# Performance work log

Measured on AMD Instinct MI355X. Metric: run time of the kernel, lower is better.

## Reference

```python
import jax, jax.numpy as jnp
import numpy as np

TWN_THRESHOLD_FACTOR = 0.05
BN_EPS = 1e-5


def ternary_quantize(w):
    # threshold = 0.05 * max|w| (detached); q in {-1, 0, +1}
    t = TWN_THRESHOLD_FACTOR * jnp.max(jnp.abs(jax.lax.stop_gradient(w)))
    return (w > t).astype(w.dtype) - (w < -t).astype(w.dtype)


def conv2d(x, w, b):
    q = ternary_quantize(w)
    y = jax.lax.conv_general_dilated(x, q, (1, 1), 'VALID',
                                     dimension_numbers=('NCHW', 'OIHW', 'NCHW'))
    return y + b[None, :, None, None]


def linear(x, w, b):
    q = ternary_quantize(w)
    return x @ q.T + b


def bn_train(x, gamma, beta, axes):
    # training-mode batch norm (biased variance), matches torch BN in train()
    mean = jnp.mean(x, axis=axes, keepdims=True)
    var = jnp.var(x, axis=axes, keepdims=True)
    xhat = (x - mean) * jax.lax.rsqrt(var + BN_EPS)
    shape = [1] * x.ndim
    shape[1] = x.shape[1]
    return xhat * gamma.reshape(shape) + beta.reshape(shape)


def maxpool2(x):
    return jax.lax.reduce_window(x, -jnp.inf, jax.lax.max,
                                 (1, 1, 2, 2), (1, 1, 2, 2), 'VALID')


def setup_inputs() -> dict:
    key = jax.random.key(0)
    ks = jax.random.split(key, 8)
    B, Cin, H, W = 512, 1, 28, 28
    C1, C2, K = 64, 128, 5
    FLAT, F1, F2 = 4 * 4 * C2, 512, 10
    inp = {
        'x': jax.random.normal(ks[0], (B, Cin, H, W), jnp.float32),
        'conv1_w': jax.random.normal(ks[1], (C1, Cin, K, K), jnp.float32) * (1.0 / np.sqrt(Cin * K * K)),
        'conv1_b': jax.random.normal(ks[2], (C1,), jnp.float32) * 0.05,
        'bn1_g': jnp.ones((C1,), jnp.float32),
        'bn1_b': jnp.zeros((C1,), jnp.float32),
        'conv2_w': jax.random.normal(ks[3], (C2, C1, K, K), jnp.float32) * (1.0 / np.sqrt(C1 * K * K)),
        'conv2_b': jax.random.normal(ks[4], (C2,), jnp.float32) * 0.05,
        'bn2_g': jnp.ones((C2,), jnp.float32),
        'bn2_b': jnp.zeros((C2,), jnp.float32),
        'fc1_w': jax.random.normal(ks[5], (F1, FLAT), jnp.float32) * (1.0 / np.sqrt(FLAT)),
        'fc1_b': jax.random.normal(ks[6], (F1,), jnp.float32) * 0.05,
        'bn3_g': jnp.ones((F1,), jnp.float32),
        'bn3_b': jnp.zeros((F1,), jnp.float32),
        'fc2_w': jax.random.normal(ks[7], (F2, F1), jnp.float32) * (1.0 / np.sqrt(F1)),
        'fc2_b': jnp.zeros((F2,), jnp.float32),
    }
    return inp


def reference(x, conv1_w, conv1_b, bn1_g, bn1_b, conv2_w, conv2_b, bn2_g, bn2_b,
              fc1_w, fc1_b, bn3_g, bn3_b, fc2_w, fc2_b):
    h = jax.nn.relu(bn_train(conv2d(x, conv1_w, conv1_b), bn1_g, bn1_b, (0, 2, 3)))
    h = maxpool2(h)  # [B, 64, 12, 12]
    h = jax.nn.relu(bn_train(conv2d(h, conv2_w, conv2_b), bn2_g, bn2_b, (0, 2, 3)))
    h = maxpool2(h)  # [B, 128, 4, 4]
    h = h.reshape(h.shape[0], -1)  # [B, 2048]
    h = jax.nn.relu(bn_train(linear(h, fc1_w, fc1_b), bn3_g, bn3_b, (0,)))
    return linear(h, fc2_w, fc2_b)  # [B, 10]
```

## Files before the change

kernel.cpp:

```cpp
#include <hip/hip_runtime.h>
#include <stdint.h>

#define EPS 1e-5f

typedef short v8s __attribute__((ext_vector_type(8)));
typedef float v4f __attribute__((ext_vector_type(4)));

static const size_t W2F   = 8192;
static const size_t WF2F  = 212992;
static const size_t A_F   = 262144;
static const size_t PMN2F = 4980736;
static const size_t B_F   = 19136512;
static const size_t WF1T  = B_F + 1048576;

#define P_C1 1024
#define P_F2 1025
#define P_C2 1040
#define P_F1 1240

__device__ inline unsigned short f2bf(float f) {
    unsigned u = __float_as_uint(f);
    return (unsigned short)((u + 0x7FFF + ((u >> 16) & 1)) >> 16);
}

__device__ __forceinline__ void stage16(const unsigned short* g, unsigned short* l) {
    __builtin_amdgcn_global_load_lds(
        (const __attribute__((address_space(1))) unsigned int*)g,
        (__attribute__((address_space(3))) unsigned int*)l, 16, 0, 0);
}

__global__ void k_absz(const float* __restrict__ c1w, const float* __restrict__ c2w,
                       const float* __restrict__ f1w, const float* __restrict__ f2w,
                       float* __restrict__ wsf) {
    __shared__ float sm4[4];
    int blk = blockIdx.x;
    if (blk >= 384) {
        if (blk < 386) {
            int i = (blk - 384) * 256 + threadIdx.x + 16;
            if (i < 528) wsf[i] = 0.f;
        } else {
            int i = (blk - 386) * 256 + threadIdx.x + 1808;
            if (i < 2832) wsf[i] = 0.f;
        }
        return;
    }
    const float* w; int n; int nb; int bi; float* out;
    if (blk == 0)       { w = c1w; n = 1600;    nb = 1;   bi = 0;         out = wsf + P_C1; }
    else if (blk == 1)  { w = f2w; n = 5120;    nb = 1;   bi = 0;         out = wsf + P_F2; }
    else if (blk < 194) { w = c2w; n = 204800;  nb = 192; bi = blk - 2;   out = wsf + P_C2 + bi; }
    else                { w = f1w; n = 1048576; nb = 190; bi = blk - 194; out = wsf + P_F1 + bi; }
    float m = 0.f;
    for (int i = bi * 256 + threadIdx.x; i < n; i += nb * 256)
        m = fmaxf(m, fabsf(w[i]));
    #pragma unroll
    for (int o = 32; o; o >>= 1) m = fmaxf(m, __shfl_down(m, o));
    if ((threadIdx.x & 63) == 0) sm4[threadIdx.x >> 6] = m;
    __syncthreads();
    if (threadIdx.x == 0)
        *out = fmaxf(fmaxf(sm4[0], sm4[1]), fmaxf(sm4[2], sm4[3]));
}

__global__ __launch_bounds__(512) void k_mid(const float* __restrict__ x,
                                             const float* __restrict__ c1w,
                                             const float* __restrict__ c2w,
                                             const float* __restrict__ f1w,
                                             const float* __restrict__ f2w,
                                             float* __restrict__ wsf,
                                             unsigned* __restrict__ pmn1,
                                             unsigned short* __restrict__ w2u,
                                             unsigned short* __restrict__ wf1,
                                             float* __restrict__ wf2) {
    int blk = blockIdx.x;
    int tid = threadIdx.x;
    if (blk >= 512) {
        if (blk < 612) {
            float m = 0.f;
            for (int i = 0; i < 192; ++i) m = fmaxf(m, wsf[P_C2 + i]);
            float t = 0.05f * m;
            for (int i = (blk - 512) * 512 + tid; i < 204800; i += 100 * 512) {
                int j    = i & 7;
                int lane = (i >> 3) & 63;
                int mt   = (i >> 9) & 7;
                int ks   = (i >> 12) & 1;
                int p    = i >> 13;
                int c  = mt * 16 + (lane & 15);
                int ci = ks * 32 + (lane >> 4) * 8 + j;
                float v = c2w[c * 1600 + ci * 25 + p];
                w2u[i] = (v > t) ? (unsigned short)0x3F80
                                 : ((v < -t) ? (unsigned short)0xBF80 : (unsigned short)0);
            }
        } else if (blk < 868) {
            float m = 0.f;
            for (int i = 0; i < 190; ++i) m = fmaxf(m, wsf[P_F1 + i]);
            float t = 0.05f * m;
            for (int i = (blk - 612) * 512 + tid; i < 1048576; i += 256 * 512) {
                float v = f1w[i];
                unsigned short q = (v > t) ? (unsigned short)0x3F80
                                 : ((v < -t) ? (unsigned short)0xBF80 : (unsigned short)0);
                int f = i >> 11, k = i & 2047;
                int ft = f >> 4, fm = f & 15;
                int ks = k >> 5, kr = k & 31;
                int lane = (kr >> 3) * 16 + fm;
                wf1[((size_t)(ks * 32 + ft) * 64 + lane) * 8 + (kr & 7)] = q;
            }
        } else {
            float t = 0.05f * wsf[P_F2];
            for (int i = tid; i < 5120; i += 512) {
                float v = f2w[i];
                wf2[i] = (float)((v > t) - (v < -t));
            }
        }
        return;
    }
    __shared__ float xs[784];
    __shared__ float red[2][8][64];
    int b = blk;
    const float4* xim = (const float4*)(x + (size_t)b * 784);
    for (int i = tid; i < 196; i += 512) ((float4*)xs)[i] = xim[i];
    int c  = tid & 63;
    int wv = tid >> 6;
    float w[25];
    {
        float t = 0.05f * wsf[P_C1];
        const float* src = c1w + c * 25;
        #pragma unroll
        for (int k = 0; k < 25; ++k) {
            float v = src[k];
            w[k] = (float)((v > t) - (v < -t));
        }
    }
    __syncthreads();
    unsigned* ob = pmn1 + (size_t)b * 9216;
    float s = 0.f, s2 = 0.f;
    int ph = 0, pw = wv;
    for (int it = 0; it < 18; ++it) {
        const float* xp = xs + (ph * 2) * 28 + pw * 2;
        float win[36];
        #pragma unroll
        for (int i = 0; i < 6; ++i)
            #pragma unroll
            for (int j = 0; j < 3; ++j) {
                float2 t2 = *(const float2*)(xp + i * 28 + j * 2);
                win[i * 6 + j * 2] = t2.x; win[i * 6 + j * 2 + 1] = t2.y;
            }
        float v00 = 0.f, v01 = 0.f, v10 = 0.f, v11 = 0.f;
        #pragma unroll
        for (int i = 0; i < 5; ++i)
            #pragma unroll
            for (int j = 0; j < 5; ++j) {
                float wk = w[i * 5 + j];
                v00 = fmaf(win[i * 6 + j],           wk, v00);
                v01 = fmaf(win[i * 6 + j + 1],       wk, v01);
                v10 = fmaf(win[(i + 1) * 6 + j],     wk, v10);
                v11 = fmaf(win[(i + 1) * 6 + j + 1], wk, v11);
            }
        s  += v00 + v01 + v10 + v11;
        s2 += v00 * v00 + v01 * v01 + v10 * v10 + v11 * v11;
        float mx = fmaxf(fmaxf(v00, v01), fmaxf(v10, v11));
        float mn = fminf(fminf(v00, v01), fminf(v10, v11));
        ob[(ph * 12 + pw) * 64 + c] = ((unsigned)f2bf(mx) << 16) | (unsigned)f2bf(mn);
        pw += 8; if (pw >= 12) { pw -= 12; ++ph; }
    }
    red[0][wv][c] = s; red[1][wv][c] = s2;
    __syncthreads();
    if (tid < 64) {
        float S = 0.f, S2 = 0.f;
        #pragma unroll
        for (int i = 0; i < 8; ++i) { S += red[0][i][tid]; S2 += red[1][i][tid]; }
        atomicAdd(&wsf[16 + tid], S);
        atomicAdd(&wsf[80 + tid], S2);
    }
}

__global__ __launch_bounds__(256) void k_conv2(const unsigned* __restrict__ pmn1,
                                               const unsigned short* __restrict__ wfrag,
                                               const float* __restrict__ c1sum,
                                               const float* __restrict__ c1ssq,
                                               const float* __restrict__ g1,
                                               const float* __restrict__ b1,
                                               float* __restrict__ pmn,
                                               float* __restrict__ sum,
                                               float* __restrict__ ssq) {
    __shared__ unsigned short xs[144 * 76];
    __shared__ unsigned short wb[3][4096];
    __shared__ float reds[2][64], redq[2][64];
    int b     = blockIdx.x >> 1;
    int mhalf = blockIdx.x & 1;
    int tid  = threadIdx.x;
    int lane = tid & 63;
    int wave = tid >> 6;
    int nh = wave & 1, kp = wave >> 1;

    int ch0 = (tid & 15) * 4;
    float scv[4], shv[4];
    {
        const float invN = 1.f / 294912.f;
        #pragma unroll
        for (int j = 0; j < 4; ++j) {
            int ch = ch0 + j;
            float mean = c1sum[ch] * invN;
            float var  = c1ssq[ch] * invN - mean * mean;
            scv[j] = g1[ch] * rsqrtf(var + EPS);
            shv[j] = b1[ch] - mean * scv[j];
        }
    }
    const uint4* srcp = (const uint4*)(pmn1 + (size_t)b * 9216);
    for (int it = 0; it < 9; ++it) {
        int i = it * 256 + tid;
        int r = i >> 4;
        uint4 u4 = srcp[i];
        unsigned long long pack = 0;
        #pragma unroll
        for (int j = 0; j < 4; ++j) {
            unsigned u = (&u4.x)[j];
            float mx = __uint_as_float(u & 0xffff0000u);
            float mn = __uint_as_float(u << 16);
            float v = (scv[j] > 0.f) ? mx : mn;
            unsigned short o = f2bf(fmaxf(0.f, fmaf(v, scv[j], shv[j])));
            pack |= ((unsigned long long)o) << (16 * j);
        }
        *(unsigned long long*)(&xs[r * 76 + ch0]) = pack;
    }
    #pragma unroll
    for (int pp = 0; pp < 2; ++pp) {
        #pragma unroll
        for (int h = 0; h < 2; ++h) {
            int ksm = wave * 2 + h;
            int ks = ksm >> 2, mt = ksm & 3;
            const unsigned short* g = wfrag +
                (size_t)((pp * 2 + ks) * 8 + mhalf * 4 + mt) * 512 + lane * 8;
            stage16(g, &wb[pp][ks * 2048 + mt * 512 + lane * 8]);
        }
    }
    __syncthreads();

    int n = lane & 15, quad = lane >> 4;
    int ow = n & 7;
    int ohb0 = nh * 4 + (n >> 3);
    int col0 = kp * 32 + quad * 8;
    v4f acc[4][2];
    #pragma unroll
    for (int mm = 0; mm < 4; ++mm) { acc[mm][0] = (v4f){0,0,0,0}; acc[mm][1] = (v4f){0,0,0,0}; }
    for (int p = 0; p < 25; ++p) {
        int cur = p % 3;
        int kh = p / 5, kw = p - (p / 5) * 5;
        int col = (ow + kw) * 76 + col0;
        v8s bf0 = *(const v8s*)(&xs[(ohb0 + kh) * 912 + col]);
        v8s bf1 = *(const v8s*)(&xs[(ohb0 + 2 + kh) * 912 + col]);
        #pragma unroll
        for (int mm = 0; mm < 4; ++mm) {
            v8s af = *(const v8s*)(&wb[cur][kp * 2048 + mm * 512 + lane * 8]);
            acc[mm][0] = __builtin_amdgcn_mfma_f32_16x16x32_bf16(af, bf0, acc[mm][0], 0, 0, 0);
            acc[mm][1] = __builtin_amdgcn_mfma_f32_16x16x32_bf16(af, bf1, acc[mm][1], 0, 0, 0);
        }
        asm volatile("s_barrier" ::: "memory");
        if (p <= 22) {
            int pn = p + 2, nxt = pn % 3;
            #pragma unroll
            for (int h = 0; h < 2; ++h) {
                int ksm = wave * 2 + h;
                int ks = ksm >> 2, mt = ksm & 3;
                const unsigned short* g = wfrag +
                    (size_t)((pn * 2 + ks) * 8 + mhalf * 4 + mt) * 512 + lane * 8;
                stage16(g, &wb[nxt][ks * 2048 + mt * 512 + lane * 8]);
            }
            asm volatile("s_waitcnt vmcnt(2)" ::: "memory");
        } else if (p == 23) {
            asm volatile("s_waitcnt vmcnt(0)" ::: "memory");
        }
        if (p <= 23)
            asm volatile("s_barrier" ::: "memory");
    }
    float* mbuf = (float*)xs;
    if (kp == 1) {
        float* d = mbuf + (nh * 64 + lane) * 36;
        #pragma unroll
        for (int mm = 0; mm < 4; ++mm) {
            *(v4f*)(d + mm * 8)     = acc[mm][0];
            *(v4f*)(d + mm * 8 + 4) = acc[mm][1];
        }
    }
    __syncthreads();
    if (kp == 0) {
        const float* s = mbuf + (nh * 64 + lane) * 36;
        #pragma unroll
        for (int mm = 0; mm < 4; ++mm) {
            acc[mm][0] += *(const v4f*)(s + mm * 8);
            acc[mm][1] += *(const v4f*)(s + mm * 8 + 4);
        }
        float* po = pmn + (size_t)b * 4096;
        #pragma unroll
        for (int mm = 0; mm < 4; ++mm) {
            int cl0 = mm * 16 + quad * 4;
            #pragma unroll
            for (int r = 0; r < 4; ++r) {
                int cl = cl0 + r;
                int cc = mhalf * 64 + cl;
                float sA = 0.f, s2A = 0.f;
                #pragma unroll
                for (int bf = 0; bf < 2; ++bf) {
                    float v = acc[mm][bf][r];
                    float pm = fmaxf(v, __shfl_xor(v, 1));
                    float pn = fminf(v, __shfl_xor(v, 1));
                    pm = fmaxf(pm, __shfl_xor(pm, 8));
                    pn = fminf(pn, __shfl_xor(pn, 8));
                    if (((n & 1) == 0) && (n < 8)) {
                        int psp = (nh * 2 + bf) * 4 + (n >> 1);
                        *(float2*)(&po[(cc * 16 + psp) * 2]) = make_float2(pm, pn);
                    }
                    float s = v, s2 = v * v;
                    #pragma unroll
                    for (int m = 1; m < 16; m <<= 1) { s += __shfl_xor(s, m); s2 += __shfl_xor(s2, m); }
                    sA += s; s2A += s2;
                }
                if (n == 0) { reds[nh][cl] = sA; redq[nh][cl] = s2A; }
            }
        }
    }
    __syncthreads();
    if (tid < 64) {
        atomicAdd(&sum[mhalf * 64 + tid], reds[0][tid] + reds[1][tid]);
        atomicAdd(&ssq[mhalf * 64 + tid], redq[0][tid] + redq[1][tid]);
    }
}

__global__ void k_bnpool2(const float* __restrict__ pmn2, const float* __restrict__ c2sum,
                          const float* __restrict__ c2ssq, const float* __restrict__ g2,
                          const float* __restrict__ b2, unsigned short* __restrict__ xfrag) {
    int i = blockIdx.x * 256 + threadIdx.x;
    int j    = i & 7;
    int lane = (i >> 3) & 63;
    int bt   = (i >> 9) & 31;
    int ks   = i >> 14;
    int b = bt * 16 + (lane & 15);
    int k = ks * 32 + (lane >> 4) * 8 + j;
    int c = k >> 4, psp = k & 15;
    float2 mm = *(const float2*)(&pmn2[((size_t)b * 2048 + c * 16 + psp) * 2]);
    float mean = c2sum[c] * (1.f / 32768.f);
    float var  = c2ssq[c] * (1.f / 32768.f) - mean * mean;
    float sc = g2[c] * rsqrtf(var + EPS);
    float sh = b2[c] - mean * sc;
    float v = (sc > 0.f) ? mm.x : mm.y;
    xfrag[i] = f2bf(fmaxf(0.f, fmaf(v, sc, sh)));
}

__global__ __launch_bounds__(256) void k_fc1(const unsigned short* __restrict__ xfrag,
                                             const unsigned short* __restrict__ wfrag,
                                             float* __restrict__ out,
                                             float* __restrict__ sum,
                                             float* __restrict__ ssq) {
    int lane = threadIdx.x & 63;
    int wave = threadIdx.x >> 6;
    int ft = (blockIdx.x & 7) * 4 + wave;
    int bT = blockIdx.x >> 3;
    v4f acc = (v4f){0.f, 0.f, 0.f, 0.f};
    for (int ks = 0; ks < 64; ++ks) {
        v8s bfrag = *(const v8s*)(xfrag + ((size_t)(ks * 32 + bT) * 64 + lane) * 8);
        v8s afrag = *(const v8s*)(wfrag + ((size_t)(ks * 32 + ft) * 64 + lane) * 8);
        acc = __builtin_amdgcn_mfma_f32_16x16x32_bf16(afrag, bfrag, acc, 0, 0, 0);
    }
    int bb = bT * 16 + (lane & 15);
    int quad = lane >> 4;
    int f0 = ft * 16 + quad * 4;
    *(float4*)(&out[(size_t)bb * 512 + f0]) =
        make_float4(acc[0], acc[1], acc[2], acc[3]);
    #pragma unroll
    for (int r = 0; r < 4; ++r) {
        float s = acc[r], s2 = s * s;
        #pragma unroll
        for (int m = 1; m < 16; m <<= 1) { s += __shfl_xor(s, m); s2 += __shfl_xor(s2, m); }
        if ((lane & 15) == 0) { atomicAdd(&sum[f0 + r], s); atomicAdd(&ssq[f0 + r], s2); }
    }
}

__global__ __launch_bounds__(256) void k_fc2(const float* __restrict__ x,
                                             const float* __restrict__ w,
                                             const float* __restrict__ bias,
                                             const float* __restrict__ fsum,
                                             const float* __restrict__ fssq,
                                             const float* __restrict__ g3,
                                             const float* __restrict__ b3,
                                             float* __restrict__ out) {
    int lane = threadIdx.x & 63;
    int b = blockIdx.x * 4 + (threadIdx.x >> 6);
    float xa[8], sm[8], sq[8], ga[8], ba[8];
    {
        const float4* p;
        p = (const float4*)(x + (size_t)b * 512 + lane * 8);
        *(float4*)xa = p[0]; *(float4*)(xa + 4) = p[1];
        p = (const float4*)(fsum + lane * 8);
        *(float4*)sm = p[0]; *(float4*)(sm + 4) = p[1];
        p = (const float4*)(fssq + lane * 8);
        *(float4*)sq = p[0]; *(float4*)(sq + 4) = p[1];
        p = (const float4*)(g3 + lane * 8);
        *(float4*)ga = p[0]; *(float4*)(ga + 4) = p[1];
        p = (const float4*)(b3 + lane * 8);
        *(float4*)ba = p[0]; *(float4*)(ba + 4) = p[1];
    }
    float h[8];
    #pragma unroll
    for (int e = 0; e < 8; ++e) {
        float mean = sm[e] * (1.f / 512.f);
        float var  = sq[e] * (1.f / 512.f) - mean * mean;
        float sc = ga[e] * rsqrtf(var + EPS);
        float sh = ba[e] - mean * sc;
        h[e] = fmaxf(0.f, fmaf(xa[e], sc, sh));
    }
    #pragma unroll
    for (int j = 0; j < 10; ++j) {
        const float4* wp = (const float4*)(w + j * 512 + lane * 8);
        float4 w0 = wp[0], w1 = wp[1];
        float p = h[0] * w0.x + h[1] * w0.y + h[2] * w0.z + h[3] * w0.w
                + h[4] * w1.x + h[5] * w1.y + h[6] * w1.z + h[7] * w1.w;
        #pragma unroll
        for (int o = 32; o; o >>= 1) p += __shfl_down(p, o);
        if (lane == 0) out[b * 10 + j] = p + bias[j];
    }
}

extern "C" void kernel_launch(void* const* d_in, const int* in_sizes, int n_in,
                              void* d_out, int out_size, void* d_ws, size_t ws_size,
                              hipStream_t stream) {
    const float* x       = (const float*)d_in[0];
    const float* conv1_w = (const float*)d_in[1];
    const float* bn1_g   = (const float*)d_in[3];
    const float* bn1_b   = (const float*)d_in[4];
    const float* conv2_w = (const float*)d_in[5];
    const float* bn2_g   = (const float*)d_in[7];
    const float* bn2_b   = (const float*)d_in[8];
    const float* fc1_w   = (const float*)d_in[9];
    const float* bn3_g   = (const float*)d_in[11];
    const float* bn3_b   = (const float*)d_in[12];
    const float* fc2_w   = (const float*)d_in[13];
    const float* fc2_b   = (const float*)d_in[14];

    float* wsf = (float*)d_ws;

    float* c1_sum = wsf + 16,   * c1_ssq = wsf + 80;
    float* c2_sum = wsf + 272,  * c2_ssq = wsf + 400;
    float* f_sum  = wsf + 1808, * f_ssq  = wsf + 2320;

    unsigned short* w2u = (unsigned short*)(wsf + W2F);
    float* wf2 = wsf + WF2F;
    unsigned short* wf1 = (unsigned short*)(wsf + WF1T);
    unsigned* PMN1 = (unsigned*)(wsf + A_F);
    float* PMN2 = wsf + PMN2F;
    float* A    = wsf + A_F;
    unsigned short* xfrag = (unsigned short*)(wsf + B_F);

    k_absz<<<390, 256, 0, stream>>>(conv1_w, conv2_w, fc1_w, fc2_w, wsf);

    k_mid<<<869, 512, 0, stream>>>(x, conv1_w, conv2_w, fc1_w, fc2_w, wsf,
                                   PMN1, w2u, wf1, wf2);

    k_conv2<<<1024, 256, 0, stream>>>(PMN1, w2u, c1_sum, c1_ssq, bn1_g, bn1_b,
                                      PMN2, c2_sum, c2_ssq);

    k_bnpool2<<<4096, 256, 0, stream>>>(PMN2, c2_sum, c2_ssq, bn2_g, bn2_b, xfrag);

    k_fc1<<<256, 256, 0, stream>>>(xfrag, wf1, A, f_sum, f_ssq);

    k_fc2<<<128, 256, 0, stream>>>(A, wf2, fc2_b, f_sum, f_ssq, bn3_g, bn3_b,
                                   (float*)d_out);
}
```

Baseline: 208.5 us.

## Process two images per conv2 block to reuse staged weight fragments

Each conv2 block now handles two batch images instead of one, so every staged weight fragment in LDS feeds twice as many MFMAs and the grid halves to 512 blocks. The weight pipeline goes from triple buffering with split barriers and explicit vmcnt waits to double buffering with a single __syncthreads per tap. The aim is to halve global weight traffic per image and the number of pipeline barriers. In exchange, LDS use and accumulator registers grow, which can lower occupancy, and the simpler prefetch exposes more load latency.

```diff
diff --git a/kernel.cpp b/kernel.cpp
--- a/kernel.cpp
+++ b/kernel.cpp
@@ -181,10 +181,10 @@
                                                float* __restrict__ pmn,
                                                float* __restrict__ sum,
                                                float* __restrict__ ssq) {
-    __shared__ unsigned short xs[144 * 76];
-    __shared__ unsigned short wb[3][4096];
+    __shared__ unsigned short xs[2][10944];
+    __shared__ unsigned short wb[2][4096];
     __shared__ float reds[2][64], redq[2][64];
-    int b     = blockIdx.x >> 1;
+    int pair  = blockIdx.x >> 1;
     int mhalf = blockIdx.x & 1;
     int tid  = threadIdx.x;
     int lane = tid & 63;
@@ -204,33 +204,33 @@
             shv[j] = b1[ch] - mean * scv[j];
         }
     }
-    const uint4* srcp = (const uint4*)(pmn1 + (size_t)b * 9216);
-    for (int it = 0; it < 9; ++it) {
-        int i = it * 256 + tid;
-        int r = i >> 4;
-        uint4 u4 = srcp[i];
-        unsigned long long pack = 0;
-        #pragma unroll
-        for (int j = 0; j < 4; ++j) {
-            unsigned u = (&u4.x)[j];
-            float mx = __uint_as_float(u & 0xffff0000u);
-            float mn = __uint_as_float(u << 16);
-            float v = (scv[j] > 0.f) ? mx : mn;
-            unsigned short o = f2bf(fmaxf(0.f, fmaf(v, scv[j], shv[j])));
-            pack |= ((unsigned long long)o) << (16 * j);
-        }
-        *(unsigned long long*)(&xs[r * 76 + ch0]) = pack;
-    }
-    #pragma unroll
-    for (int pp = 0; pp < 2; ++pp) {
-        #pragma unroll
-        for (int h = 0; h < 2; ++h) {
-            int ksm = wave * 2 + h;
-            int ks = ksm >> 2, mt = ksm & 3;
-            const unsigned short* g = wfrag +
-                (size_t)((pp * 2 + ks) * 8 + mhalf * 4 + mt) * 512 + lane * 8;
-            stage16(g, &wb[pp][ks * 2048 + mt * 512 + lane * 8]);
-        }
+    #pragma unroll
+    for (int ii = 0; ii < 2; ++ii) {
+        const uint4* srcp = (const uint4*)(pmn1 + (size_t)(pair * 2 + ii) * 9216);
+        unsigned short* xsi = &xs[ii][0];
+        for (int it = 0; it < 9; ++it) {
+            int i = it * 256 + tid;
+            int r = i >> 4;
+            uint4 u4 = srcp[i];
+            unsigned long long pack = 0;
+            #pragma unroll
+            for (int j = 0; j < 4; ++j) {
+                unsigned u = (&u4.x)[j];
+                float mx = __uint_as_float(u & 0xffff0000u);
+                float mn = __uint_as_float(u << 16);
+                float v = (scv[j] > 0.f) ? mx : mn;
+                unsigned short o = f2bf(fmaxf(0.f, fmaf(v, scv[j], shv[j])));
+                pack |= ((unsigned long long)o) << (16 * j);
+            }
+            *(unsigned long long*)(&xsi[r * 76 + ch0]) = pack;
+        }
+    }
+    #pragma unroll
+    for (int h = 0; h < 2; ++h) {
+        int ksm = wave * 2 + h;
+        int ks = ksm >> 2, mt = ksm & 3;
+        const unsigned short* g = wfrag + (size_t)(ks * 8 + mhalf * 4 + mt) * 512 + lane * 8;
+        stage16(g, &wb[0][ks * 2048 + mt * 512 + lane * 8]);
     }
     __syncthreads();
 
@@ -238,57 +238,67 @@
     int ow = n & 7;
     int ohb0 = nh * 4 + (n >> 3);
     int col0 = kp * 32 + quad * 8;
-    v4f acc[4][2];
-    #pragma unroll
-    for (int mm = 0; mm < 4; ++mm) { acc[mm][0] = (v4f){0,0,0,0}; acc[mm][1] = (v4f){0,0,0,0}; }
+    v4f acc[2][4][2];
+    #pragma unroll
+    for (int ii = 0; ii < 2; ++ii)
+        #pragma unroll
+        for (int mm = 0; mm < 4; ++mm) {
+            acc[ii][mm][0] = (v4f){0,0,0,0};
+            acc[ii][mm][1] = (v4f){0,0,0,0};
+        }
     for (int p = 0; p < 25; ++p) {
-        int cur = p % 3;
-        int kh = p / 5, kw = p - (p / 5) * 5;
-        int col = (ow + kw) * 76 + col0;
-        v8s bf0 = *(const v8s*)(&xs[(ohb0 + kh) * 912 + col]);
-        v8s bf1 = *(const v8s*)(&xs[(ohb0 + 2 + kh) * 912 + col]);
-        #pragma unroll
-        for (int mm = 0; mm < 4; ++mm) {
-            v8s af = *(const v8s*)(&wb[cur][kp * 2048 + mm * 512 + lane * 8]);
-            acc[mm][0] = __builtin_amdgcn_mfma_f32_16x16x32_bf16(af, bf0, acc[mm][0], 0, 0, 0);
-            acc[mm][1] = __builtin_amdgcn_mfma_f32_16x16x32_bf16(af, bf1, acc[mm][1], 0, 0, 0);
-        }
-        asm volatile("s_barrier" ::: "memory");
-        if (p <= 22) {
-            int pn = p + 2, nxt = pn % 3;
+        int cur = p & 1;
+        if (p < 24) {
             #pragma unroll
             for (int h = 0; h < 2; ++h) {
                 int ksm = wave * 2 + h;
                 int ks = ksm >> 2, mt = ksm & 3;
                 const unsigned short* g = wfrag +
-                    (size_t)((pn * 2 + ks) * 8 + mhalf * 4 + mt) * 512 + lane * 8;
-                stage16(g, &wb[nxt][ks * 2048 + mt * 512 + lane * 8]);
-            }
-            asm volatile("s_waitcnt vmcnt(2)" ::: "memory");
-        } else if (p == 23) {
-            asm volatile("s_waitcnt vmcnt(0)" ::: "memory");
-        }
-        if (p <= 23)
-            asm volatile("s_barrier" ::: "memory");
+                    (size_t)(((p + 1) * 2 + ks) * 8 + mhalf * 4 + mt) * 512 + lane * 8;
+                stage16(g, &wb[cur ^ 1][ks * 2048 + mt * 512 + lane * 8]);
+            }
+        }
+        int kh = p / 5, kw = p - (p / 5) * 5;
+        int col = (ow + kw) * 76 + col0;
+        v8s bfA0 = *(const v8s*)(&xs[0][(ohb0 + kh) * 912 + col]);
+        v8s bfA1 = *(const v8s*)(&xs[0][(ohb0 + 2 + kh) * 912 + col]);
+        v8s bfB0 = *(const v8s*)(&xs[1][(ohb0 + kh) * 912 + col]);
+        v8s bfB1 = *(const v8s*)(&xs[1][(ohb0 + 2 + kh) * 912 + col]);
+        #pragma unroll
+        for (int mm = 0; mm < 4; ++mm) {
+            v8s af = *(const v8s*)(&wb[cur][kp * 2048 + mm * 512 + lane * 8]);
+            acc[0][mm][0] = __builtin_amdgcn_mfma_f32_16x16x32_bf16(af, bfA0, acc[0][mm][0], 0, 0, 0);
+            acc[0][mm][1] = __builtin_amdgcn_mfma_f32_16x16x32_bf16(af, bfA1, acc[0][mm][1], 0, 0, 0);
+            acc[1][mm][0] = __builtin_amdgcn_mfma_f32_16x16x32_bf16(af, bfB0, acc[1][mm][0], 0, 0, 0);
+            acc[1][mm][1] = __builtin_amdgcn_mfma_f32_16x16x32_bf16(af, bfB1, acc[1][mm][1], 0, 0, 0);
+        }
+        __syncthreads();
     }
     float* mbuf = (float*)xs;
     if (kp == 1) {
-        float* d = mbuf + (nh * 64 + lane) * 36;
-        #pragma unroll
-        for (int mm = 0; mm < 4; ++mm) {
-            *(v4f*)(d + mm * 8)     = acc[mm][0];
-            *(v4f*)(d + mm * 8 + 4) = acc[mm][1];
+        #pragma unroll
+        for (int ii = 0; ii < 2; ++ii) {
+            float* d = mbuf + ii * 4608 + (nh * 64 + lane) * 36;
+            #pragma unroll
+            for (int mm = 0; mm < 4; ++mm) {
+                *(v4f*)(d + mm * 8)     = acc[ii][mm][0];
+                *(v4f*)(d + mm * 8 + 4) = acc[ii][mm][1];
+            }
         }
     }
     __syncthreads();
     if (kp == 0) {
-        const float* s = mbuf + (nh * 64 + lane) * 36;
-        #pragma unroll
-        for (int mm = 0; mm < 4; ++mm) {
-            acc[mm][0] += *(const v4f*)(s + mm * 8);
-            acc[mm][1] += *(const v4f*)(s + mm * 8 + 4);
-        }
-        float* po = pmn + (size_t)b * 4096;
+        #pragma unroll
+        for (int ii = 0; ii < 2; ++ii) {
+            const float* s = mbuf + ii * 4608 + (nh * 64 + lane) * 36;
+            #pragma unroll
+            for (int mm = 0; mm < 4; ++mm) {
+                acc[ii][mm][0] += *(const v4f*)(s + mm * 8);
+                acc[ii][mm][1] += *(const v4f*)(s + mm * 8 + 4);
+            }
+        }
+        float* po0 = pmn + (size_t)(pair * 2 + 0) * 4096;
+        float* po1 = pmn + (size_t)(pair * 2 + 1) * 4096;
         #pragma unroll
         for (int mm = 0; mm < 4; ++mm) {
             int cl0 = mm * 16 + quad * 4;
@@ -298,20 +308,24 @@
                 int cc = mhalf * 64 + cl;
                 float sA = 0.f, s2A = 0.f;
                 #pragma unroll
-                for (int bf = 0; bf < 2; ++bf) {
-                    float v = acc[mm][bf][r];
-                    float pm = fmaxf(v, __shfl_xor(v, 1));
-                    float pn = fminf(v, __shfl_xor(v, 1));
-                    pm = fmaxf(pm, __shfl_xor(pm, 8));
-                    pn = fminf(pn, __shfl_xor(pn, 8));
-                    if (((n & 1) == 0) && (n < 8)) {
-                        int psp = (nh * 2 + bf) * 4 + (n >> 1);
-                        *(float2*)(&po[(cc * 16 + psp) * 2]) = make_float2(pm, pn);
+                for (int ii = 0; ii < 2; ++ii) {
+                    float* po = ii ? po1 : po0;
+                    #pragma unroll
+                    for (int bf = 0; bf < 2; ++bf) {
+                        float v = acc[ii][mm][bf][r];
+                        float pm = fmaxf(v, __shfl_xor(v, 1));
+                        float pn = fminf(v, __shfl_xor(v, 1));
+                        pm = fmaxf(pm, __shfl_xor(pm, 8));
+                        pn = fminf(pn, __shfl_xor(pn, 8));
+                        if (((n & 1) == 0) && (n < 8)) {
+                            int psp = (nh * 2 + bf) * 4 + (n >> 1);
+                            *(float2*)(&po[(cc * 16 + psp) * 2]) = make_float2(pm, pn);
+                        }
+                        float s = v, s2 = v * v;
+                        #pragma unroll
+                        for (int m = 1; m < 16; m <<= 1) { s += __shfl_xor(s, m); s2 += __shfl_xor(s2, m); }
+                        sA += s; s2A += s2;
                     }
-                    float s = v, s2 = v * v;
-                    #pragma unroll
-                    for (int m = 1; m < 16; m <<= 1) { s += __shfl_xor(s, m); s2 += __shfl_xor(s2, m); }
-                    sA += s; s2A += s2;
                 }
                 if (n == 0) { reds[nh][cl] = sA; redq[nh][cl] = s2A; }
             }
@@ -453,8 +467,8 @@
     k_mid<<<869, 512, 0, stream>>>(x, conv1_w, conv2_w, fc1_w, fc2_w, wsf,
                                    PMN1, w2u, wf1, wf2);
 
-    k_conv2<<<1024, 256, 0, stream>>>(PMN1, w2u, c1_sum, c1_ssq, bn1_g, bn1_b,
-                                      PMN2, c2_sum, c2_ssq);
+    k_conv2<<<512, 256, 0, stream>>>(PMN1, w2u, c1_sum, c1_ssq, bn1_g, bn1_b,
+                                     PMN2, c2_sum, c2_ssq);
 
     k_bnpool2<<<4096, 256, 0, stream>>>(PMN2, c2_sum, c2_ssq, bn2_g, bn2_b, xfrag);
 
```

Result: faster. 199.5 us (-4.3%).
